# Optimization experiments

Hardware: AMD Instinct MI355X
Metric: run time of the kernel (lower is better)

Reference implementation:

```python
import jax, jax.numpy as jnp
import numpy as np

N = 50000      # nodes
E = 800000     # edges
HID = 64       # hidden_dim
HEADS = 4
DH = HID // HEADS
PIN = 128      # person_in_dim
DIN = 64       # disease_in_dim
NEXP = 4       # num_experts
K = 2          # topk
L = 2          # n_layers
NEG = 0.2      # gat_neg_slope


def setup_inputs() -> dict:
    key = jax.random.key(0)
    ks = iter(jax.random.split(key, 64))
    nrm = lambda shp, s=0.05: jax.random.normal(next(ks), shp, jnp.float32) * s
    d = {}
    d["features"] = jax.random.normal(next(ks), (N, PIN), jnp.float32)
    d["node_types"] = jax.random.randint(next(ks), (N,), 0, 2)
    d["src"] = jax.random.randint(next(ks), (E,), 0, N)
    d["dst"] = jax.random.randint(next(ks), (E,), 0, N)
    d["W_person"] = nrm((PIN, HID)); d["b_person"] = jnp.zeros((HID,), jnp.float32)
    d["W_disease"] = nrm((DIN, HID)); d["b_disease"] = jnp.zeros((HID,), jnp.float32)
    d["gat_W"] = nrm((L, HID, HID)); d["gat_al"] = nrm((L, HEADS, DH)); d["gat_ar"] = nrm((L, HEADS, DH))
    d["gin_eps"] = jnp.zeros((L,), jnp.float32)
    d["gin_W1"] = nrm((L, HID, HID)); d["gin_b1"] = jnp.zeros((L, HID), jnp.float32)
    d["gin_W2"] = nrm((L, HID, HID)); d["gin_b2"] = jnp.zeros((L, HID), jnp.float32)
    for p in ("gat", "gin"):
        d[p + "_gW"] = nrm((HID, NEXP)); d[p + "_gb"] = jnp.zeros((NEXP,), jnp.float32)
        d[p + "_eW1"] = nrm((NEXP, HID, HID // 2)); d[p + "_eb1"] = jnp.zeros((NEXP, HID // 2), jnp.float32)
        d[p + "_eW2"] = nrm((NEXP, HID // 2, HID)); d[p + "_eb2"] = jnp.zeros((NEXP, HID), jnp.float32)
    d["fg_W1"] = nrm((2 * HID, HID)); d["fg_b1"] = jnp.zeros((HID,), jnp.float32)
    d["fg_W2"] = nrm((HID, HID)); d["fg_b2"] = jnp.zeros((HID,), jnp.float32)
    return d


def _edge_softmax(logits, dst):
    m = jax.ops.segment_max(logits, dst, num_segments=N)
    e = jnp.exp(logits - m[dst])
    s = jax.ops.segment_sum(e, dst, num_segments=N)
    return e / (s[dst] + 1e-9)


def _gat(h, src, dst, gat_W, gat_al, gat_ar):
    for l in range(L):
        hW = (h @ gat_W[l]).reshape(N, HEADS, DH)
        el = (hW * gat_al[l]).sum(-1)                    # [N, HEADS]
        er = (hW * gat_ar[l]).sum(-1)
        lg = jax.nn.leaky_relu(el[src] + er[dst], NEG)   # [E, HEADS]
        a = _edge_softmax(lg, dst)
        out = jax.ops.segment_sum(hW[src] * a[:, :, None], dst, num_segments=N)
        h2 = out.reshape(N, HID) + h                     # residual=True
        h = jax.nn.relu(h2) if l < L - 1 else h2
    return h


def _gin(h, src, dst, gin_eps, gin_W1, gin_b1, gin_W2, gin_b2):
    deg = jax.ops.segment_sum(jnp.ones((E,), jnp.float32), dst, num_segments=N)
    inv = 1.0 / jnp.maximum(deg, 1.0)
    for l in range(L):
        agg = jax.ops.segment_sum(h[src], dst, num_segments=N) * inv[:, None]  # 'mean' aggregator
        x = (1.0 + gin_eps[l]) * h + agg                 # learn_eps=True
        x = jax.nn.relu(x @ gin_W1[l] + gin_b1[l]) @ gin_W2[l] + gin_b2[l]     # 2-layer MLP
        h = jax.nn.relu(x) if l < L - 1 else x
    return h


def _expert(h, gW, gb, eW1, eb1, eW2, eb2):
    probs = jax.nn.softmax(h @ gW + gb, axis=-1)         # [N, NEXP]
    topv, topi = jax.lax.top_k(probs, K)
    topv = topv / topv.sum(-1, keepdims=True)
    hot = jax.nn.one_hot(topi, NEXP, dtype=h.dtype)      # [N, K, NEXP]
    w = (hot * topv[..., None]).sum(1)                   # [N, NEXP] sparse weights
    e1 = jax.nn.relu(jnp.einsum('nd,edh->neh', h, eW1) + eb1)
    e2 = jnp.einsum('neh,ehd->ned', e1, eW2) + eb2       # [N, NEXP, HID]
    out = (e2 * w[:, :, None]).sum(1)
    f = hot.sum(1).mean(0)                               # routed fraction per expert
    P = probs.mean(0)
    aux = NEXP * jnp.sum(f * P)                          # switch-style load balancing
    return out, aux


def reference(features, node_types, src, dst, W_person, b_person, W_disease, b_disease,
              gat_W, gat_al, gat_ar, gin_eps, gin_W1, gin_b1, gin_W2, gin_b2,
              gat_gW, gat_gb, gat_eW1, gat_eb1, gat_eW2, gat_eb2,
              gin_gW, gin_gb, gin_eW1, gin_eb1, gin_eW2, gin_eb2,
              fg_W1, fg_b1, fg_W2, fg_b2):
    # per-type projection + scatter into shared buffer
    hp = features[:, :PIN] @ W_person + b_person
    hd = features[:, :DIN] @ W_disease + b_disease
    h = jnp.where((node_types == 0)[:, None], hp, hd)
    z_gat = _gat(h, src, dst, gat_W, gat_al, gat_ar)
    z_gin = _gin(h, src, dst, gin_eps, gin_W1, gin_b1, gin_W2, gin_b2)
    zg, aux_g = _expert(z_gat, gat_gW, gat_gb, gat_eW1, gat_eb1, gat_eW2, gat_eb2)
    zi, aux_i = _expert(z_gin, gin_gW, gin_gb, gin_eW1, gin_eb1, gin_eW2, gin_eb2)
    z = zi * zg
    u = jnp.concatenate([zg, zi], axis=-1)
    gate = jax.nn.sigmoid(jax.nn.relu(u @ fg_W1 + fg_b1) @ fg_W2 + fg_b2)
    u_prime = gate  # source calls fusion_gate(u) twice -> identical deterministic value
    z = gate * z + (1.0 - gate) * u_prime
    return z, aux_i + aux_g
```

## Files before the change

kernel.cpp:

```cpp
#include <hip/hip_runtime.h>

#define NN 50000
#define EE 800000
#define NEG 0.2f
#define NBG 391
#define NBE 196
#define NBKT 391
#define EPB 4096
#define NSEG 196

typedef __attribute__((ext_vector_type(8))) short s8;
typedef __attribute__((ext_vector_type(4))) float f4;

__device__ __forceinline__ float leaky(float x) { return x > 0.f ? x : NEG * x; }
__device__ __forceinline__ unsigned bf16r(float x) {
    unsigned u = __float_as_uint(x);
    return (u + 0x7fffu + ((u >> 16) & 1u)) >> 16;
}
__device__ __forceinline__ float lo16(unsigned p) { return __uint_as_float(p << 16); }
__device__ __forceinline__ float hi16(unsigned p) { return __uint_as_float(p & 0xffff0000u); }

__device__ __forceinline__ s8 a_from_f32(const float* p) {
    float4 u = *reinterpret_cast<const float4*>(p);
    float4 v = *reinterpret_cast<const float4*>(p + 4);
    s8 r;
    r[0] = (short)bf16r(u.x); r[1] = (short)bf16r(u.y);
    r[2] = (short)bf16r(u.z); r[3] = (short)bf16r(u.w);
    r[4] = (short)bf16r(v.x); r[5] = (short)bf16r(v.y);
    r[6] = (short)bf16r(v.z); r[7] = (short)bf16r(v.w);
    return r;
}

__global__ __launch_bounds__(256) void k_binA_pre(
        const int* __restrict__ src, const int* __restrict__ dst,
        int* __restrict__ seg_off, int* __restrict__ seg_cnt,
        unsigned* __restrict__ gseg, int* __restrict__ bucket_tot,
        const float* __restrict__ feat, const int* __restrict__ types,
        const float* __restrict__ Wp, const float* __restrict__ bp,
        const float* __restrict__ Wd, const float* __restrict__ bd,
        const float* __restrict__ gW, const float* __restrict__ al,
        const float* __restrict__ ar,
        float* __restrict__ h0f, unsigned* __restrict__ P,
        float* __restrict__ el, float* __restrict__ er) {
    __shared__ unsigned short WpT[64 * 136];
    __shared__ unsigned short WdT[64 * 72];
    __shared__ unsigned short WgT[64 * 72];
    __shared__ unsigned short y0s[4][16 * 72];
    if (blockIdx.x < NSEG) {
        unsigned* sbuf = (unsigned*)WpT;
        int* cnt = (int*)WdT;
        int* pre = (int*)WgT;
        int* ssc = (int*)y0s;
        for (int i = threadIdx.x; i < NBKT; i += 256) cnt[i] = 0;
        __syncthreads();
        int e0 = blockIdx.x * EPB;
        int nE = EE - e0; if (nE > EPB) nE = EPB;
        int b[16]; unsigned val[16]; int rk[16];
        #pragma unroll
        for (int i = 0; i < 16; i++) {
            int li = i * 256 + threadIdx.x;
            if (li < nE) {
                int e = e0 + li;
                int d = dst[e], s = src[e];
                b[i] = d >> 7;
                val[i] = ((unsigned)s << 7) | (unsigned)(d & 127);
                rk[i] = atomicAdd(&cnt[b[i]], 1);
            } else b[i] = -1;
        }
        __syncthreads();
        int t = threadIdx.x;
        int c0 = (2 * t     < NBKT) ? cnt[2 * t]     : 0;
        int c1 = (2 * t + 1 < NBKT) ? cnt[2 * t + 1] : 0;
        ssc[t] = c0 + c1;
        __syncthreads();
        for (int off = 1; off < 256; off <<= 1) {
            int u = (t >= off) ? ssc[t - off] : 0;
            __syncthreads();
            ssc[t] += u;
            __syncthreads();
        }
        int base = ssc[t] - (c0 + c1);
        pre[2 * t] = base;
        pre[2 * t + 1] = base + c0;
        __syncthreads();
        #pragma unroll
        for (int i = 0; i < 16; i++)
            if (b[i] >= 0) sbuf[pre[b[i]] + rk[i]] = val[i];
        for (int i = t; i < NBKT; i += 256) {
            seg_off[blockIdx.x * NBKT + i] = pre[i];
            seg_cnt[blockIdx.x * NBKT + i] = cnt[i];
            atomicAdd(&bucket_tot[i], cnt[i]);
        }
        __syncthreads();
        for (int i = t; i < nE; i += 256)
            gseg[(size_t)blockIdx.x * EPB + i] = sbuf[i];
        return;
    }
    for (int idx = threadIdx.x; idx < 128 * 64; idx += 256) {
        int k = idx >> 6, n = idx & 63;
        WpT[n * 136 + k] = (unsigned short)bf16r(Wp[idx]);
    }
    for (int idx = threadIdx.x; idx < 64 * 64; idx += 256) {
        int k = idx >> 6, n = idx & 63;
        WdT[n * 72 + k] = (unsigned short)bf16r(Wd[idx]);
        WgT[n * 72 + k] = (unsigned short)bf16r(gW[idx]);
    }
    __syncthreads();
    int wv = threadIdx.x >> 6, lane = threadIdx.x & 63;
    int quad = lane >> 4, l16 = lane & 15;
    int gw2 = (blockIdx.x - NSEG) * 4 + wv;
    int mtEnd = gw2 * 2 + 2; if (mtEnd > 3125) mtEnd = 3125;
    for (int mt = gw2 * 2; mt < mtEnd; mt++) {
        int row0 = mt * 16;
        const float* arow = feat + (size_t)(row0 + l16) * 128;
        f4 accp[4], accd[4];
        #pragma unroll
        for (int t = 0; t < 4; t++) { accp[t] = f4{0.f,0.f,0.f,0.f}; accd[t] = f4{0.f,0.f,0.f,0.f}; }
        #pragma unroll
        for (int ks = 0; ks < 4; ks++) {
            s8 a = a_from_f32(arow + ks * 32 + quad * 8);
            #pragma unroll
            for (int t = 0; t < 4; t++) {
                s8 b = *(const s8*)&WpT[(t * 16 + l16) * 136 + ks * 32 + quad * 8];
                accp[t] = __builtin_amdgcn_mfma_f32_16x16x32_bf16(a, b, accp[t], 0, 0, 0);
                if (ks < 2) {
                    s8 bd_ = *(const s8*)&WdT[(t * 16 + l16) * 72 + ks * 32 + quad * 8];
                    accd[t] = __builtin_amdgcn_mfma_f32_16x16x32_bf16(a, bd_, accd[t], 0, 0, 0);
                }
            }
        }
        int ty[4];
        #pragma unroll
        for (int r = 0; r < 4; r++) ty[r] = types[row0 + quad * 4 + r];
        float vv[4][4];
        #pragma unroll
        for (int t = 0; t < 4; t++) {
            int col = t * 16 + l16;
            float bpv = bp[col], bdv = bd[col];
            #pragma unroll
            for (int r = 0; r < 4; r++) {
                float v = ty[r] ? (accd[t][r] + bdv) : (accp[t][r] + bpv);
                vv[t][r] = v;
                h0f[(size_t)(row0 + quad * 4 + r) * 64 + col] = v;
                y0s[wv][(quad * 4 + r) * 72 + col] = (unsigned short)bf16r(v);
            }
        }
        s8 a0 = *(const s8*)&y0s[wv][l16 * 72 + quad * 8];
        s8 a1 = *(const s8*)&y0s[wv][l16 * 72 + 32 + quad * 8];
        f4 hw[4];
        #pragma unroll
        for (int t = 0; t < 4; t++) {
            hw[t] = f4{0.f,0.f,0.f,0.f};
            s8 b0 = *(const s8*)&WgT[(t * 16 + l16) * 72 + quad * 8];
            hw[t] = __builtin_amdgcn_mfma_f32_16x16x32_bf16(a0, b0, hw[t], 0, 0, 0);
            s8 b1_ = *(const s8*)&WgT[(t * 16 + l16) * 72 + 32 + quad * 8];
            hw[t] = __builtin_amdgcn_mfma_f32_16x16x32_bf16(a1, b1_, hw[t], 0, 0, 0);
        }
        #pragma unroll
        for (int t = 0; t < 4; t++) {
            int col = t * 16 + l16;
            float alv = al[col], arv = ar[col];
            #pragma unroll
            for (int r = 0; r < 4; r++) {
                int row = row0 + quad * 4 + r;
                float h = hw[t][r];
                P[(size_t)row * 64 + col] = bf16r(h) | (bf16r(vv[t][r]) << 16);
                float pl = h * alv, pr = h * arv;
                #pragma unroll
                for (int m = 1; m < 16; m <<= 1) {
                    pl += __shfl_xor(pl, m, 64);
                    pr += __shfl_xor(pr, m, 64);
                }
                if (l16 == 0) {
                    el[(size_t)row * 4 + t] = pl;
                    er[(size_t)row * 4 + t] = pr;
                }
            }
        }
    }
}

__global__ __launch_bounds__(256) void k_binB(
        int* __restrict__ row_start, const int* __restrict__ seg_off,
        const int* __restrict__ seg_cnt, const unsigned* __restrict__ gseg,
        int* __restrict__ csr_src, const int* __restrict__ bucket_tot) {
    __shared__ int spre[256];
    __shared__ int soff[NSEG];
    __shared__ int ss[256];
    __shared__ int kur[128];
    __shared__ int sred[4];
    int b = blockIdx.x;
    int t = threadIdx.x;
    int bt = 0;
    for (int i = t; i < b; i += 256) bt += bucket_tot[i];
    #pragma unroll
    for (int o2 = 1; o2 < 64; o2 <<= 1) bt += __shfl_xor(bt, o2, 64);
    if ((t & 63) == 0) sred[t >> 6] = bt;
    int c0 = (t < NSEG) ? seg_cnt[t * NBKT + b] : 0;
    if (t < NSEG) soff[t] = seg_off[t * NBKT + b];
    ss[t] = c0;
    __syncthreads();
    int bstart = sred[0] + sred[1] + sred[2] + sred[3];
    for (int off = 1; off < 256; off <<= 1) {
        int u = (t >= off) ? ss[t - off] : 0;
        __syncthreads();
        ss[t] += u;
        __syncthreads();
    }
    spre[t] = ss[t] - c0;
    int cntb = ss[255];
    if (t < 128) kur[t] = 0;
    __syncthreads();
    for (int idx = t; idx < cntb; idx += 256) {
        int lo = 0, hi = 255;
        #pragma unroll
        for (int s = 0; s < 8; s++) {
            int mid = (lo + hi + 1) >> 1;
            if (spre[mid] <= idx) lo = mid; else hi = mid - 1;
        }
        unsigned v = gseg[(size_t)lo * EPB + soff[lo] + (idx - spre[lo])];
        atomicAdd(&kur[v & 127], 1);
    }
    __syncthreads();
    int deg = (t < 128) ? kur[t] : 0;
    ss[t] = deg;
    __syncthreads();
    for (int off = 1; off < 256; off <<= 1) {
        int u = (t >= off) ? ss[t - off] : 0;
        __syncthreads();
        ss[t] += u;
        __syncthreads();
    }
    if (t < 128) {
        int cur = bstart + ss[t] - deg;
        kur[t] = cur;
        int d = (b << 7) + t;
        if (d < NN) row_start[d] = cur;
    }
    if (b == 0 && t == 0) row_start[NN] = EE;
    __syncthreads();
    for (int idx = t; idx < cntb; idx += 256) {
        int lo = 0, hi = 255;
        #pragma unroll
        for (int s = 0; s < 8; s++) {
            int mid = (lo + hi + 1) >> 1;
            if (spre[mid] <= idx) lo = mid; else hi = mid - 1;
        }
        unsigned v = gseg[(size_t)lo * EPB + soff[lo] + (idx - spre[lo])];
        int p = atomicAdd(&kur[v & 127], 1);
        csr_src[p] = (int)(v >> 7);
    }
}

template <int RELU>
__global__ void k_edges(const int* __restrict__ rows, const int* __restrict__ csr,
                        const unsigned* __restrict__ Pin,
                        const float* __restrict__ el, const float* __restrict__ er,
                        const float* __restrict__ gat_in, const float* __restrict__ gin_in,
                        const float* __restrict__ eps_p,
                        float* __restrict__ vgf, unsigned short* __restrict__ vgb,
                        unsigned short* __restrict__ xb) {
    __shared__ float ews[4][256];
    int wv = threadIdx.x >> 6, lane = threadIdx.x & 63;
    int n = blockIdx.x * 4 + wv;
    int st = rows[n], dg = rows[n + 1] - st;
    int hd = lane >> 4;
    float4 erv = *reinterpret_cast<const float4*>(er + (size_t)n * 4);
    float accg = 0.f, acci = 0.f, ssum = 0.f;
    for (int base = 0; base < dg; base += 64) {
        int rem = dg - base; if (rem > 64) rem = 64;
        int myi = 0;
        if (lane < rem) {
            myi = csr[st + base + lane];
            float4 lv = *reinterpret_cast<const float4*>(el + (size_t)myi * 4);
            float4 ev;
            ev.x = __expf(leaky(lv.x + erv.x));
            ev.y = __expf(leaky(lv.y + erv.y));
            ev.z = __expf(leaky(lv.z + erv.z));
            ev.w = __expf(leaky(lv.w + erv.w));
            *reinterpret_cast<float4*>(&ews[wv][lane * 4]) = ev;
        }
        int j = 0;
        for (; j + 4 <= rem; j += 4) {
            int s0 = __shfl(myi, j, 64),     s1 = __shfl(myi, j + 1, 64);
            int s2 = __shfl(myi, j + 2, 64), s3 = __shfl(myi, j + 3, 64);
            unsigned p0 = Pin[(size_t)s0 * 64 + lane];
            unsigned p1 = Pin[(size_t)s1 * 64 + lane];
            unsigned p2 = Pin[(size_t)s2 * 64 + lane];
            unsigned p3 = Pin[(size_t)s3 * 64 + lane];
            float a0 = ews[wv][(j + 0) * 4 + hd];
            float a1 = ews[wv][(j + 1) * 4 + hd];
            float a2 = ews[wv][(j + 2) * 4 + hd];
            float a3 = ews[wv][(j + 3) * 4 + hd];
            accg += a0 * lo16(p0) + a1 * lo16(p1) + a2 * lo16(p2) + a3 * lo16(p3);
            acci += hi16(p0) + hi16(p1) + hi16(p2) + hi16(p3);
            ssum += a0 + a1 + a2 + a3;
        }
        for (; j < rem; j++) {
            int s0 = __shfl(myi, j, 64);
            unsigned p0 = Pin[(size_t)s0 * 64 + lane];
            float a0 = ews[wv][j * 4 + hd];
            accg += a0 * lo16(p0); acci += hi16(p0); ssum += a0;
        }
    }
    float vg = accg / (ssum + 1e-9f) + gat_in[(size_t)n * 64 + lane];
    if (RELU) vg = fmaxf(vg, 0.f);
    float invd = 1.0f / fmaxf((float)dg, 1.0f);
    float x = (1.0f + eps_p[0]) * gin_in[(size_t)n * 64 + lane] + acci * invd;
    size_t off = (size_t)n * 64 + lane;
    vgf[off] = vg;
    vgb[off] = (unsigned short)bf16r(vg);
    xb[off] = (unsigned short)bf16r(x);
}

template <int L>
__global__ __launch_bounds__(256) void k_mlp(const unsigned short* __restrict__ Gx,
        const unsigned short* __restrict__ Eb,
        const float* __restrict__ W1, const float* __restrict__ b1,
        const float* __restrict__ W2, const float* __restrict__ b2,
        const float* __restrict__ gatW, const float* __restrict__ al,
        const float* __restrict__ ar,
        unsigned short* __restrict__ Fb, float* __restrict__ Cf,
        unsigned* __restrict__ P, float* __restrict__ el, float* __restrict__ er,
        const float* __restrict__ Zg, const float* __restrict__ ggW,
        const float* __restrict__ ggb, const float* __restrict__ igW,
        const float* __restrict__ igb,
        float* __restrict__ wgtg, float* __restrict__ wgti,
        float* __restrict__ stats) {
    __shared__ unsigned short W1T[64 * 72];
    __shared__ unsigned short W2T[64 * 72];
    __shared__ unsigned short WgT[(L == 0) ? 64 * 72 : 64];
    __shared__ unsigned short y1s[4][16 * 72];
    __shared__ float sstat[16];
    if (L == 1 && threadIdx.x < 16) sstat[threadIdx.x] = 0.f;
    for (int idx = threadIdx.x; idx < 64 * 64; idx += 256) {
        int k = idx >> 6, n = idx & 63;
        W1T[n * 72 + k] = (unsigned short)bf16r(W1[idx]);
        W2T[n * 72 + k] = (unsigned short)bf16r(W2[idx]);
        if (L == 0) WgT[n * 72 + k] = (unsigned short)bf16r(gatW[idx]);
    }
    __syncthreads();
    int wv = threadIdx.x >> 6, lane = threadIdx.x & 63;
    int quad = lane >> 4, l16 = lane & 15;
    int gw = blockIdx.x * 4 + wv;
    int mtEnd = gw * 2 + 2; if (mtEnd > 3125) mtEnd = 3125;
    float sp[2][4] = {{0,0,0,0},{0,0,0,0}};
    float sh[2][4] = {{0,0,0,0},{0,0,0,0}};
    for (int mt = gw * 2; mt < mtEnd; mt++) {
        int row0 = mt * 16;
        const unsigned short* arow = Gx + (size_t)(row0 + l16) * 64;
        s8 a0 = *(const s8*)(arow + quad * 8);
        s8 a1 = *(const s8*)(arow + 32 + quad * 8);
        f4 acc1[4];
        #pragma unroll
        for (int t = 0; t < 4; t++) {
            acc1[t] = f4{0.f,0.f,0.f,0.f};
            s8 b0 = *(const s8*)&W1T[(t * 16 + l16) * 72 + quad * 8];
            acc1[t] = __builtin_amdgcn_mfma_f32_16x16x32_bf16(a0, b0, acc1[t], 0, 0, 0);
            s8 b1_ = *(const s8*)&W1T[(t * 16 + l16) * 72 + 32 + quad * 8];
            acc1[t] = __builtin_amdgcn_mfma_f32_16x16x32_bf16(a1, b1_, acc1[t], 0, 0, 0);
        }
        #pragma unroll
        for (int t = 0; t < 4; t++) {
            float b1v = b1[t * 16 + l16];
            #pragma unroll
            for (int r = 0; r < 4; r++) {
                float v = fmaxf(acc1[t][r] + b1v, 0.f);
                y1s[wv][(quad * 4 + r) * 72 + t * 16 + l16] = (unsigned short)bf16r(v);
            }
        }
        s8 c0 = *(const s8*)&y1s[wv][l16 * 72 + quad * 8];
        s8 c1 = *(const s8*)&y1s[wv][l16 * 72 + 32 + quad * 8];
        f4 acc2[4];
        #pragma unroll
        for (int t = 0; t < 4; t++) {
            acc2[t] = f4{0.f,0.f,0.f,0.f};
            s8 b0 = *(const s8*)&W2T[(t * 16 + l16) * 72 + quad * 8];
            acc2[t] = __builtin_amdgcn_mfma_f32_16x16x32_bf16(c0, b0, acc2[t], 0, 0, 0);
            s8 b1_ = *(const s8*)&W2T[(t * 16 + l16) * 72 + 32 + quad * 8];
            acc2[t] = __builtin_amdgcn_mfma_f32_16x16x32_bf16(c1, b1_, acc2[t], 0, 0, 0);
        }
        unsigned short vb[4][4];
        float vout[4][4];
        #pragma unroll
        for (int t = 0; t < 4; t++) {
            int col = t * 16 + l16;
            float b2v = b2[col];
            #pragma unroll
            for (int r = 0; r < 4; r++) {
                float v = acc2[t][r] + b2v;
                if (L == 0) v = fmaxf(v, 0.f);
                size_t off = (size_t)(row0 + quad * 4 + r) * 64 + col;
                unsigned short vb16 = (unsigned short)bf16r(v);
                vb[t][r] = vb16;
                vout[t][r] = v;
                Fb[off] = vb16;
                if (L == 0) Cf[off] = v;
            }
        }
        if (L == 0) {
            const unsigned short* erow = Eb + (size_t)(row0 + l16) * 64;
            s8 e0 = *(const s8*)(erow + quad * 8);
            s8 e1 = *(const s8*)(erow + 32 + quad * 8);
            f4 hw[4];
            #pragma unroll
            for (int t = 0; t < 4; t++) {
                hw[t] = f4{0.f,0.f,0.f,0.f};
                s8 b0 = *(const s8*)&WgT[(t * 16 + l16) * 72 + quad * 8];
                hw[t] = __builtin_amdgcn_mfma_f32_16x16x32_bf16(e0, b0, hw[t], 0, 0, 0);
                s8 b1_ = *(const s8*)&WgT[(t * 16 + l16) * 72 + 32 + quad * 8];
                hw[t] = __builtin_amdgcn_mfma_f32_16x16x32_bf16(e1, b1_, hw[t], 0, 0, 0);
            }
            #pragma unroll
            for (int t = 0; t < 4; t++) {
                int col = t * 16 + l16;
                float alv = al[col], arv = ar[col];
                #pragma unroll
                for (int r = 0; r < 4; r++) {
                    int row = row0 + quad * 4 + r;
                    float h = hw[t][r];
                    P[(size_t)row * 64 + col] = bf16r(h) | ((unsigned)vb[t][r] << 16);
                    float pl = h * alv, pr = h * arv;
                    #pragma unroll
                    for (int m = 1; m < 16; m <<= 1) {
                        pl += __shfl_xor(pl, m, 64);
                        pr += __shfl_xor(pr, m, 64);
                    }
                    if (l16 == 0) {
                        el[(size_t)row * 4 + t] = pl;
                        er[(size_t)row * 4 + t] = pr;
                    }
                }
            }
        } else {
            #pragma unroll
            for (int r = 0; r < 4; r++) {
                int row = row0 + quad * 4 + r;
                float pg[4] = {0,0,0,0}, pi[4] = {0,0,0,0};
                #pragma unroll
                for (int t = 0; t < 4; t++) {
                    int col = t * 16 + l16;
                    float zgv = Zg[(size_t)row * 64 + col];
                    float ziv = vout[t][r];
                    #pragma unroll
                    for (int e = 0; e < 4; e++) {
                        pg[e] += zgv * ggW[col * 4 + e];
                        pi[e] += ziv * igW[col * 4 + e];
                    }
                }
                #pragma unroll
                for (int m = 1; m < 16; m <<= 1) {
                    #pragma unroll
                    for (int e = 0; e < 4; e++) {
                        pg[e] += __shfl_xor(pg[e], m, 64);
                        pi[e] += __shfl_xor(pi[e], m, 64);
                    }
                }
                if (l16 == 0) {
                    #pragma unroll
                    for (int q = 0; q < 2; q++) {
                        float lg0 = (q ? pi[0] + igb[0] : pg[0] + ggb[0]);
                        float lg1 = (q ? pi[1] + igb[1] : pg[1] + ggb[1]);
                        float lg2 = (q ? pi[2] + igb[2] : pg[2] + ggb[2]);
                        float lg3 = (q ? pi[3] + igb[3] : pg[3] + ggb[3]);
                        float mx = fmaxf(fmaxf(lg0, lg1), fmaxf(lg2, lg3));
                        float ex0 = __expf(lg0 - mx), ex1 = __expf(lg1 - mx);
                        float ex2 = __expf(lg2 - mx), ex3 = __expf(lg3 - mx);
                        float inv = 1.0f / (ex0 + ex1 + ex2 + ex3);
                        float pr4[4] = {ex0 * inv, ex1 * inv, ex2 * inv, ex3 * inv};
                        int i1 = 0; float v1 = pr4[0];
                        #pragma unroll
                        for (int t = 1; t < 4; t++) if (pr4[t] > v1) { v1 = pr4[t]; i1 = t; }
                        int i2 = -1; float v2 = -1.f;
                        #pragma unroll
                        for (int t = 0; t < 4; t++) if (t != i1 && pr4[t] > v2) { v2 = pr4[t]; i2 = t; }
                        float wsum = v1 + v2;
                        float wq[4] = {0.f, 0.f, 0.f, 0.f};
                        wq[i1] = v1 / wsum; wq[i2] = v2 / wsum;
                        float* WD = q ? wgti : wgtg;
                        *reinterpret_cast<float4*>(WD + (size_t)row * 4) =
                            float4{wq[0], wq[1], wq[2], wq[3]};
                        #pragma unroll
                        for (int t = 0; t < 4; t++) sp[q][t] += pr4[t];
                        sh[q][i1] += 1.f; sh[q][i2] += 1.f;
                    }
                }
            }
        }
    }
    if (L == 1) {
        __syncthreads();
        if (l16 == 0) {
            #pragma unroll
            for (int q = 0; q < 2; q++)
                #pragma unroll
                for (int e = 0; e < 4; e++) {
                    atomicAdd(&sstat[q * 8 + e], sp[q][e]);
                    atomicAdd(&sstat[q * 8 + 4 + e], sh[q][e]);
                }
        }
        __syncthreads();
        if (threadIdx.x < 16) atomicAdd(&stats[threadIdx.x], sstat[threadIdx.x]);
    }
}

__global__ __launch_bounds__(256) void k_expert(const unsigned short* __restrict__ Eb,
        const unsigned short* __restrict__ Fb,
        const float* __restrict__ g_eW1, const float* __restrict__ g_eb1,
        const float* __restrict__ g_eW2, const float* __restrict__ g_eb2,
        const float* __restrict__ i_eW1, const float* __restrict__ i_eb1,
        const float* __restrict__ i_eW2, const float* __restrict__ i_eb2,
        const float* __restrict__ wgtg, const float* __restrict__ wgti,
        float* __restrict__ moegf, float* __restrict__ moeif,
        unsigned short* __restrict__ ub) {
    __shared__ unsigned short w1t[4 * 32 * 72];
    __shared__ unsigned short w2t[4 * 64 * 40];
    __shared__ unsigned short y1s[4][16 * 40];
    int p = (blockIdx.x >= NBE) ? 1 : 0;
    int bb = blockIdx.x - p * NBE;
    const unsigned short* Ab = p ? Fb : Eb;
    const float* eW1 = p ? i_eW1 : g_eW1;
    const float* eb1 = p ? i_eb1 : g_eb1;
    const float* eW2 = p ? i_eW2 : g_eW2;
    const float* eb2 = p ? i_eb2 : g_eb2;
    const float* wgt = p ? wgti : wgtg;
    float* moef = p ? moeif : moegf;
    int qoff = p ? 64 : 0;
    for (int g = threadIdx.x; g < 8192; g += 256) {
        int e = g >> 11, rem = g & 2047;
        int k = rem >> 5, n = rem & 31;
        w1t[e * 2304 + n * 72 + k] = (unsigned short)bf16r(eW1[g]);
    }
    for (int g = threadIdx.x; g < 8192; g += 256) {
        int e = g >> 11, rem = g & 2047;
        int k = rem >> 6, n = rem & 63;
        w2t[e * 2560 + n * 40 + k] = (unsigned short)bf16r(eW2[g]);
    }
    __syncthreads();
    int wv = threadIdx.x >> 6, lane = threadIdx.x & 63;
    int quad = lane >> 4, l16 = lane & 15;
    int gw = bb * 4 + wv;
    int mtEnd = gw * 4 + 4; if (mtEnd > 3125) mtEnd = 3125;
    for (int mt = gw * 4; mt < mtEnd; mt++) {
        int row0 = mt * 16;
        const unsigned short* arow = Ab + (size_t)(row0 + l16) * 64;
        s8 a0 = *(const s8*)(arow + quad * 8);
        s8 a1 = *(const s8*)(arow + 32 + quad * 8);
        f4 outacc[4];
        #pragma unroll
        for (int t = 0; t < 4; t++) outacc[t] = f4{0.f,0.f,0.f,0.f};
        for (int e = 0; e < 4; e++) {
            f4 acc1[2];
            #pragma unroll
            for (int t = 0; t < 2; t++) {
                acc1[t] = f4{0.f,0.f,0.f,0.f};
                s8 b0 = *(const s8*)&w1t[e * 2304 + (t * 16 + l16) * 72 + quad * 8];
                acc1[t] = __builtin_amdgcn_mfma_f32_16x16x32_bf16(a0, b0, acc1[t], 0, 0, 0);
                s8 b1_ = *(const s8*)&w1t[e * 2304 + (t * 16 + l16) * 72 + 32 + quad * 8];
                acc1[t] = __builtin_amdgcn_mfma_f32_16x16x32_bf16(a1, b1_, acc1[t], 0, 0, 0);
            }
            #pragma unroll
            for (int t = 0; t < 2; t++) {
                float b1v = eb1[e * 32 + t * 16 + l16];
                #pragma unroll
                for (int r = 0; r < 4; r++) {
                    float v = fmaxf(acc1[t][r] + b1v, 0.f);
                    y1s[wv][(quad * 4 + r) * 40 + t * 16 + l16] = (unsigned short)bf16r(v);
                }
            }
            s8 a2 = *(const s8*)&y1s[wv][l16 * 40 + quad * 8];
            f4 acc2[4];
            #pragma unroll
            for (int t = 0; t < 4; t++) {
                acc2[t] = f4{0.f,0.f,0.f,0.f};
                s8 b2_ = *(const s8*)&w2t[e * 2560 + (t * 16 + l16) * 40 + quad * 8];
                acc2[t] = __builtin_amdgcn_mfma_f32_16x16x32_bf16(a2, b2_, acc2[t], 0, 0, 0);
            }
            #pragma unroll
            for (int t = 0; t < 4; t++) {
                float b2v = eb2[e * 64 + t * 16 + l16];
                #pragma unroll
                for (int r = 0; r < 4; r++) {
                    float we = wgt[(size_t)(row0 + quad * 4 + r) * 4 + e];
                    outacc[t][r] += we * (acc2[t][r] + b2v);
                }
            }
        }
        #pragma unroll
        for (int t = 0; t < 4; t++) {
            int col = t * 16 + l16;
            #pragma unroll
            for (int r = 0; r < 4; r++) {
                int row = row0 + quad * 4 + r;
                float v = outacc[t][r];
                moef[(size_t)row * 64 + col] = v;
                ub[(size_t)row * 128 + qoff + col] = (unsigned short)bf16r(v);
            }
        }
    }
}

__global__ __launch_bounds__(256) void k_fusion(const unsigned short* __restrict__ ubuf,
        const float* __restrict__ W1, const float* __restrict__ b1,
        const float* __restrict__ W2, const float* __restrict__ b2,
        const float* __restrict__ moegf, const float* __restrict__ moeif,
        float* __restrict__ out, const float* __restrict__ stats) {
    __shared__ unsigned short W1T[64 * 136];
    __shared__ unsigned short W2T[64 * 72];
    __shared__ unsigned short y1s[4][16 * 72];
    for (int idx = threadIdx.x; idx < 128 * 64; idx += 256) {
        int k = idx >> 6, n = idx & 63;
        W1T[n * 136 + k] = (unsigned short)bf16r(W1[idx]);
    }
    for (int idx = threadIdx.x; idx < 64 * 64; idx += 256) {
        int k = idx >> 6, n = idx & 63;
        W2T[n * 72 + k] = (unsigned short)bf16r(W2[idx]);
    }
    __syncthreads();
    int wv = threadIdx.x >> 6, lane = threadIdx.x & 63;
    int quad = lane >> 4, l16 = lane & 15;
    int gw = blockIdx.x * 4 + wv;
    int mtEnd = gw * 2 + 2; if (mtEnd > 3125) mtEnd = 3125;
    for (int mt = gw * 2; mt < mtEnd; mt++) {
        int row0 = mt * 16;
        const unsigned short* arow = ubuf + (size_t)(row0 + l16) * 128;
        f4 acc1[4];
        #pragma unroll
        for (int t = 0; t < 4; t++) acc1[t] = f4{0.f,0.f,0.f,0.f};
        #pragma unroll
        for (int ks = 0; ks < 4; ks++) {
            s8 a = *(const s8*)(arow + ks * 32 + quad * 8);
            #pragma unroll
            for (int t = 0; t < 4; t++) {
                s8 b = *(const s8*)&W1T[(t * 16 + l16) * 136 + ks * 32 + quad * 8];
                acc1[t] = __builtin_amdgcn_mfma_f32_16x16x32_bf16(a, b, acc1[t], 0, 0, 0);
            }
        }
        #pragma unroll
        for (int t = 0; t < 4; t++) {
            float b1v = b1[t * 16 + l16];
            #pragma unroll
            for (int r = 0; r < 4; r++) {
                float v = fmaxf(acc1[t][r] + b1v, 0.f);
                y1s[wv][(quad * 4 + r) * 72 + t * 16 + l16] = (unsigned short)bf16r(v);
            }
        }
        f4 acc2[4];
        #pragma unroll
        for (int t = 0; t < 4; t++) acc2[t] = f4{0.f,0.f,0.f,0.f};
        #pragma unroll
        for (int ks = 0; ks < 2; ks++) {
            s8 a = *(const s8*)&y1s[wv][l16 * 72 + ks * 32 + quad * 8];
            #pragma unroll
            for (int t = 0; t < 4; t++) {
                s8 b = *(const s8*)&W2T[(t * 16 + l16) * 72 + ks * 32 + quad * 8];
                acc2[t] = __builtin_amdgcn_mfma_f32_16x16x32_bf16(a, b, acc2[t], 0, 0, 0);
            }
        }
        #pragma unroll
        for (int t = 0; t < 4; t++) {
            int col = t * 16 + l16;
            float b2v = b2[col];
            #pragma unroll
            for (int r = 0; r < 4; r++) {
                int row = row0 + quad * 4 + r;
                float g = 1.0f / (1.0f + __expf(-(acc2[t][r] + b2v)));
                float zgv = moegf[(size_t)row * 64 + col];
                float ziv = moeif[(size_t)row * 64 + col];
                out[(size_t)row * 64 + col] = g * zgv * ziv + (1.0f - g) * g;
            }
        }
    }
    if (blockIdx.x == 0 && threadIdx.x < 64) {
        int t = threadIdx.x;
        float s = (t < 16) ? stats[t] : 0.f;
        float aux = 0.f;
        for (int q = 0; q < 2; q++) {
            float a = 0.f;
            for (int e = 0; e < 4; e++) {
                float pr = __shfl(s, q * 8 + e, 64);
                float f  = __shfl(s, q * 8 + 4 + e, 64);
                a += (f / (float)NN) * (pr / (float)NN);
            }
            aux += 4.0f * a;
        }
        if (t == 0) out[(size_t)NN * 64] = aux;
    }
}

extern "C" void kernel_launch(void* const* d_in, const int* in_sizes, int n_in,
                              void* d_out, int out_size, void* d_ws, size_t ws_size,
                              hipStream_t stream) {
    (void)in_sizes; (void)n_in; (void)out_size; (void)ws_size;
    const float* features  = (const float*)d_in[0];
    const int*   node_types= (const int*)d_in[1];
    const int*   src       = (const int*)d_in[2];
    const int*   dst       = (const int*)d_in[3];
    const float* W_person  = (const float*)d_in[4];
    const float* b_person  = (const float*)d_in[5];
    const float* W_disease = (const float*)d_in[6];
    const float* b_disease = (const float*)d_in[7];
    const float* gat_W     = (const float*)d_in[8];
    const float* gat_al    = (const float*)d_in[9];
    const float* gat_ar    = (const float*)d_in[10];
    const float* gin_eps   = (const float*)d_in[11];
    const float* gin_W1    = (const float*)d_in[12];
    const float* gin_b1    = (const float*)d_in[13];
    const float* gin_W2    = (const float*)d_in[14];
    const float* gin_b2    = (const float*)d_in[15];
    const float* gat_gW    = (const float*)d_in[16];
    const float* gat_gb    = (const float*)d_in[17];
    const float* gat_eW1   = (const float*)d_in[18];
    const float* gat_eb1   = (const float*)d_in[19];
    const float* gat_eW2   = (const float*)d_in[20];
    const float* gat_eb2   = (const float*)d_in[21];
    const float* gin_gW    = (const float*)d_in[22];
    const float* gin_gb    = (const float*)d_in[23];
    const float* gin_eW1   = (const float*)d_in[24];
    const float* gin_eb1   = (const float*)d_in[25];
    const float* gin_eW2   = (const float*)d_in[26];
    const float* gin_eb2   = (const float*)d_in[27];
    const float* fg_W1     = (const float*)d_in[28];
    const float* fg_b1     = (const float*)d_in[29];
    const float* fg_W2     = (const float*)d_in[30];
    const float* fg_b2     = (const float*)d_in[31];
    float* out = (float*)d_out;

    float* ws = (float*)d_ws;
    size_t o = 0;
    float* A = ws + o; o += (size_t)NN * 64;
    float* B = ws + o; o += (size_t)NN * 64;
    float* C = ws + o; o += (size_t)NN * 64;
    unsigned short* E  = (unsigned short*)(ws + o); o += (size_t)NN * 32;
    unsigned short* F  = (unsigned short*)(ws + o); o += (size_t)NN * 32;
    unsigned short* G  = (unsigned short*)(ws + o); o += (size_t)NN * 32;
    unsigned* P = (unsigned*)(ws + o); o += (size_t)NN * 64;
    float* el = ws + o; o += (size_t)NN * 4;
    float* er = ws + o; o += (size_t)NN * 4;
    float* wgtg = ws + o; o += (size_t)NN * 4;
    float* wgti = ws + o; o += (size_t)NN * 4;
    int* bucket_tot = (int*)(ws + o); o += 392;
    float* stats    = ws + o; o += 16;
    int* row_start = (int*)(ws + o); o += NN + 4;
    int* csr_src   = (int*)(ws + o); o += EE;
    int* seg_off   = (int*)(ws + o); o += NSEG * NBKT + 64;
    int* seg_cnt   = (int*)(ws + o); o += NSEG * NBKT + 64;
    unsigned* gseg = (unsigned*)(ws + o); o += (size_t)NSEG * EPB;

    unsigned short* ub = (unsigned short*)A;

    const int NB_node = NN / 4;

    hipMemsetAsync(bucket_tot, 0, sizeof(int) * 392 + sizeof(float) * 16, stream);

    k_binA_pre<<<NSEG + NBG, 256, 0, stream>>>(src, dst, seg_off, seg_cnt, gseg, bucket_tot,
                                               features, node_types, W_person, b_person,
                                               W_disease, b_disease, gat_W, gat_al, gat_ar,
                                               A, P, el, er);

    k_binB<<<NBKT, 256, 0, stream>>>(row_start, seg_off, seg_cnt, gseg, csr_src, bucket_tot);

    k_edges<1><<<NB_node, 256, 0, stream>>>(row_start, csr_src, P, el, er, A, A,
                                            gin_eps, B, E, G);
    k_mlp<0><<<NBG, 256, 0, stream>>>(G, E, gin_W1, gin_b1, gin_W2, gin_b2,
                                      gat_W + 4096, gat_al + 64, gat_ar + 64,
                                      F, C, P, el, er,
                                      nullptr, nullptr, nullptr, nullptr, nullptr,
                                      nullptr, nullptr, nullptr);

    k_edges<0><<<NB_node, 256, 0, stream>>>(row_start, csr_src, P, el, er, B, C,
                                            gin_eps + 1, B, E, G);
    k_mlp<1><<<NBG, 256, 0, stream>>>(G, nullptr, gin_W1 + 4096, gin_b1 + 64,
                                      gin_W2 + 4096, gin_b2 + 64,
                                      nullptr, nullptr, nullptr,
                                      F, nullptr, nullptr, nullptr, nullptr,
                                      B, gat_gW, gat_gb, gin_gW, gin_gb,
                                      wgtg, wgti, stats);

    k_expert<<<NBE * 2, 256, 0, stream>>>(E, F,
                                          gat_eW1, gat_eb1, gat_eW2, gat_eb2,
                                          gin_eW1, gin_eb1, gin_eW2, gin_eb2,
                                          wgtg, wgti, B, C, ub);

    k_fusion<<<NBG, 256, 0, stream>>>(ub, fg_W1, fg_b1, fg_W2, fg_b2, B, C, out, stats);
}
```

Before: 320.3 us.

## Fuse MoE expert and fusion-gate kernels into one tail kernel

Merges the expert kernel and the fusion-gate kernel into a single launch. Each wave computes both experts' outputs for its two row tiles, keeps them in registers, and writes only the bf16 concatenation buffer, which the same wave reads back for the gate MLP. This removes one launch and the fp32 round trip of the expert outputs through global memory. In exchange, each block now converts all three weight sets into shared memory in turn, which adds barriers and more per-block setup work, and it raises register pressure from holding the expert accumulators.

```diff
diff --git a/kernel.cpp b/kernel.cpp
--- a/kernel.cpp
+++ b/kernel.cpp
@@ -4,7 +4,7 @@
 #define EE 800000
 #define NEG 0.2f
 #define NBG 391
-#define NBE 196
+#define NBT 392
 #define NBKT 391
 #define EPB 4096
 #define NSEG 196
@@ -504,170 +504,169 @@
     }
 }
 
-__global__ __launch_bounds__(256) void k_expert(const unsigned short* __restrict__ Eb,
+__global__ __launch_bounds__(256) void k_tail(const unsigned short* __restrict__ Eb,
         const unsigned short* __restrict__ Fb,
         const float* __restrict__ g_eW1, const float* __restrict__ g_eb1,
         const float* __restrict__ g_eW2, const float* __restrict__ g_eb2,
         const float* __restrict__ i_eW1, const float* __restrict__ i_eb1,
         const float* __restrict__ i_eW2, const float* __restrict__ i_eb2,
         const float* __restrict__ wgtg, const float* __restrict__ wgti,
-        float* __restrict__ moegf, float* __restrict__ moeif,
-        unsigned short* __restrict__ ub) {
-    __shared__ unsigned short w1t[4 * 32 * 72];
-    __shared__ unsigned short w2t[4 * 64 * 40];
-    __shared__ unsigned short y1s[4][16 * 40];
-    int p = (blockIdx.x >= NBE) ? 1 : 0;
-    int bb = blockIdx.x - p * NBE;
-    const unsigned short* Ab = p ? Fb : Eb;
-    const float* eW1 = p ? i_eW1 : g_eW1;
-    const float* eb1 = p ? i_eb1 : g_eb1;
-    const float* eW2 = p ? i_eW2 : g_eW2;
-    const float* eb2 = p ? i_eb2 : g_eb2;
-    const float* wgt = p ? wgti : wgtg;
-    float* moef = p ? moeif : moegf;
-    int qoff = p ? 64 : 0;
-    for (int g = threadIdx.x; g < 8192; g += 256) {
-        int e = g >> 11, rem = g & 2047;
-        int k = rem >> 5, n = rem & 31;
-        w1t[e * 2304 + n * 72 + k] = (unsigned short)bf16r(eW1[g]);
-    }
-    for (int g = threadIdx.x; g < 8192; g += 256) {
-        int e = g >> 11, rem = g & 2047;
-        int k = rem >> 6, n = rem & 63;
-        w2t[e * 2560 + n * 40 + k] = (unsigned short)bf16r(eW2[g]);
-    }
-    __syncthreads();
-    int wv = threadIdx.x >> 6, lane = threadIdx.x & 63;
-    int quad = lane >> 4, l16 = lane & 15;
-    int gw = bb * 4 + wv;
-    int mtEnd = gw * 4 + 4; if (mtEnd > 3125) mtEnd = 3125;
-    for (int mt = gw * 4; mt < mtEnd; mt++) {
-        int row0 = mt * 16;
-        const unsigned short* arow = Ab + (size_t)(row0 + l16) * 64;
-        s8 a0 = *(const s8*)(arow + quad * 8);
-        s8 a1 = *(const s8*)(arow + 32 + quad * 8);
-        f4 outacc[4];
-        #pragma unroll
-        for (int t = 0; t < 4; t++) outacc[t] = f4{0.f,0.f,0.f,0.f};
-        for (int e = 0; e < 4; e++) {
-            f4 acc1[2];
-            #pragma unroll
-            for (int t = 0; t < 2; t++) {
-                acc1[t] = f4{0.f,0.f,0.f,0.f};
-                s8 b0 = *(const s8*)&w1t[e * 2304 + (t * 16 + l16) * 72 + quad * 8];
-                acc1[t] = __builtin_amdgcn_mfma_f32_16x16x32_bf16(a0, b0, acc1[t], 0, 0, 0);
-                s8 b1_ = *(const s8*)&w1t[e * 2304 + (t * 16 + l16) * 72 + 32 + quad * 8];
-                acc1[t] = __builtin_amdgcn_mfma_f32_16x16x32_bf16(a1, b1_, acc1[t], 0, 0, 0);
-            }
-            #pragma unroll
-            for (int t = 0; t < 2; t++) {
-                float b1v = eb1[e * 32 + t * 16 + l16];
-                #pragma unroll
-                for (int r = 0; r < 4; r++) {
-                    float v = fmaxf(acc1[t][r] + b1v, 0.f);
-                    y1s[wv][(quad * 4 + r) * 40 + t * 16 + l16] = (unsigned short)bf16r(v);
-                }
-            }
-            s8 a2 = *(const s8*)&y1s[wv][l16 * 40 + quad * 8];
-            f4 acc2[4];
-            #pragma unroll
-            for (int t = 0; t < 4; t++) {
-                acc2[t] = f4{0.f,0.f,0.f,0.f};
-                s8 b2_ = *(const s8*)&w2t[e * 2560 + (t * 16 + l16) * 40 + quad * 8];
-                acc2[t] = __builtin_amdgcn_mfma_f32_16x16x32_bf16(a2, b2_, acc2[t], 0, 0, 0);
-            }
-            #pragma unroll
-            for (int t = 0; t < 4; t++) {
-                float b2v = eb2[e * 64 + t * 16 + l16];
-                #pragma unroll
-                for (int r = 0; r < 4; r++) {
-                    float we = wgt[(size_t)(row0 + quad * 4 + r) * 4 + e];
-                    outacc[t][r] += we * (acc2[t][r] + b2v);
-                }
-            }
-        }
-        #pragma unroll
-        for (int t = 0; t < 4; t++) {
-            int col = t * 16 + l16;
-            #pragma unroll
-            for (int r = 0; r < 4; r++) {
-                int row = row0 + quad * 4 + r;
-                float v = outacc[t][r];
-                moef[(size_t)row * 64 + col] = v;
-                ub[(size_t)row * 128 + qoff + col] = (unsigned short)bf16r(v);
-            }
-        }
-    }
-}
-
-__global__ __launch_bounds__(256) void k_fusion(const unsigned short* __restrict__ ubuf,
         const float* __restrict__ W1, const float* __restrict__ b1,
         const float* __restrict__ W2, const float* __restrict__ b2,
-        const float* __restrict__ moegf, const float* __restrict__ moeif,
-        float* __restrict__ out, const float* __restrict__ stats) {
-    __shared__ unsigned short W1T[64 * 136];
-    __shared__ unsigned short W2T[64 * 72];
+        unsigned short* __restrict__ ub, float* __restrict__ out,
+        const float* __restrict__ stats) {
+    __shared__ unsigned short wbuf[4 * 32 * 72 + 4 * 64 * 40];
     __shared__ unsigned short y1s[4][16 * 72];
-    for (int idx = threadIdx.x; idx < 128 * 64; idx += 256) {
-        int k = idx >> 6, n = idx & 63;
-        W1T[n * 136 + k] = (unsigned short)bf16r(W1[idx]);
-    }
-    for (int idx = threadIdx.x; idx < 64 * 64; idx += 256) {
-        int k = idx >> 6, n = idx & 63;
-        W2T[n * 72 + k] = (unsigned short)bf16r(W2[idx]);
-    }
-    __syncthreads();
     int wv = threadIdx.x >> 6, lane = threadIdx.x & 63;
     int quad = lane >> 4, l16 = lane & 15;
     int gw = blockIdx.x * 4 + wv;
-    int mtEnd = gw * 2 + 2; if (mtEnd > 3125) mtEnd = 3125;
-    for (int mt = gw * 2; mt < mtEnd; mt++) {
-        int row0 = mt * 16;
-        const unsigned short* arow = ubuf + (size_t)(row0 + l16) * 128;
-        f4 acc1[4];
-        #pragma unroll
-        for (int t = 0; t < 4; t++) acc1[t] = f4{0.f,0.f,0.f,0.f};
-        #pragma unroll
-        for (int ks = 0; ks < 4; ks++) {
-            s8 a = *(const s8*)(arow + ks * 32 + quad * 8);
+    int mt0 = gw * 2;
+    f4 moe[2][2][4];
+    #pragma unroll
+    for (int p = 0; p < 2; p++)
+        #pragma unroll
+        for (int m = 0; m < 2; m++)
+            #pragma unroll
+            for (int t = 0; t < 4; t++) moe[p][m][t] = f4{0.f,0.f,0.f,0.f};
+    #pragma unroll
+    for (int p = 0; p < 2; p++) {
+        const unsigned short* Ab = p ? Fb : Eb;
+        const float* eW1 = p ? i_eW1 : g_eW1;
+        const float* eb1 = p ? i_eb1 : g_eb1;
+        const float* eW2 = p ? i_eW2 : g_eW2;
+        const float* eb2 = p ? i_eb2 : g_eb2;
+        const float* wgt = p ? wgti : wgtg;
+        int qoff = p ? 64 : 0;
+        if (p) __syncthreads();
+        for (int g = threadIdx.x; g < 8192; g += 256) {
+            int e = g >> 11, rem = g & 2047;
+            int k = rem >> 5, n = rem & 31;
+            wbuf[e * 2304 + n * 72 + k] = (unsigned short)bf16r(eW1[g]);
+        }
+        for (int g = threadIdx.x; g < 8192; g += 256) {
+            int e = g >> 11, rem = g & 2047;
+            int k = rem >> 6, n = rem & 63;
+            wbuf[9216 + e * 2560 + n * 40 + k] = (unsigned short)bf16r(eW2[g]);
+        }
+        __syncthreads();
+        #pragma unroll
+        for (int m = 0; m < 2; m++) {
+            int mt = mt0 + m;
+            if (mt < 3125) {
+                int row0 = mt * 16;
+                const unsigned short* arow = Ab + (size_t)(row0 + l16) * 64;
+                s8 a0 = *(const s8*)(arow + quad * 8);
+                s8 a1 = *(const s8*)(arow + 32 + quad * 8);
+                for (int e = 0; e < 4; e++) {
+                    f4 acc1[2];
+                    #pragma unroll
+                    for (int t = 0; t < 2; t++) {
+                        acc1[t] = f4{0.f,0.f,0.f,0.f};
+                        s8 b0 = *(const s8*)&wbuf[e * 2304 + (t * 16 + l16) * 72 + quad * 8];
+                        acc1[t] = __builtin_amdgcn_mfma_f32_16x16x32_bf16(a0, b0, acc1[t], 0, 0, 0);
+                        s8 b1_ = *(const s8*)&wbuf[e * 2304 + (t * 16 + l16) * 72 + 32 + quad * 8];
+                        acc1[t] = __builtin_amdgcn_mfma_f32_16x16x32_bf16(a1, b1_, acc1[t], 0, 0, 0);
+                    }
+                    #pragma unroll
+                    for (int t = 0; t < 2; t++) {
+                        float b1v = eb1[e * 32 + t * 16 + l16];
+                        #pragma unroll
+                        for (int r = 0; r < 4; r++) {
+                            float v = fmaxf(acc1[t][r] + b1v, 0.f);
+                            y1s[wv][(quad * 4 + r) * 40 + t * 16 + l16] = (unsigned short)bf16r(v);
+                        }
+                    }
+                    s8 a2 = *(const s8*)&y1s[wv][l16 * 40 + quad * 8];
+                    f4 acc2[4];
+                    #pragma unroll
+                    for (int t = 0; t < 4; t++) {
+                        acc2[t] = f4{0.f,0.f,0.f,0.f};
+                        s8 b2_ = *(const s8*)&wbuf[9216 + e * 2560 + (t * 16 + l16) * 40 + quad * 8];
+                        acc2[t] = __builtin_amdgcn_mfma_f32_16x16x32_bf16(a2, b2_, acc2[t], 0, 0, 0);
+                    }
+                    #pragma unroll
+                    for (int t = 0; t < 4; t++) {
+                        float b2v = eb2[e * 64 + t * 16 + l16];
+                        #pragma unroll
+                        for (int r = 0; r < 4; r++) {
+                            float we = wgt[(size_t)(row0 + quad * 4 + r) * 4 + e];
+                            moe[p][m][t][r] += we * (acc2[t][r] + b2v);
+                        }
+                    }
+                }
+                #pragma unroll
+                for (int t = 0; t < 4; t++) {
+                    int col = t * 16 + l16;
+                    #pragma unroll
+                    for (int r = 0; r < 4; r++) {
+                        int row = row0 + quad * 4 + r;
+                        ub[(size_t)row * 128 + qoff + col] = (unsigned short)bf16r(moe[p][m][t][r]);
+                    }
+                }
+            }
+        }
+    }
+    __syncthreads();
+    for (int idx = threadIdx.x; idx < 128 * 64; idx += 256) {
+        int k = idx >> 6, n = idx & 63;
+        wbuf[n * 136 + k] = (unsigned short)bf16r(W1[idx]);
+    }
+    for (int idx = threadIdx.x; idx < 64 * 64; idx += 256) {
+        int k = idx >> 6, n = idx & 63;
+        wbuf[8704 + n * 72 + k] = (unsigned short)bf16r(W2[idx]);
+    }
+    __syncthreads();
+    #pragma unroll
+    for (int m = 0; m < 2; m++) {
+        int mt = mt0 + m;
+        if (mt < 3125) {
+            int row0 = mt * 16;
+            const unsigned short* arow = ub + (size_t)(row0 + l16) * 128;
+            f4 acc1[4];
+            #pragma unroll
+            for (int t = 0; t < 4; t++) acc1[t] = f4{0.f,0.f,0.f,0.f};
+            #pragma unroll
+            for (int ks = 0; ks < 4; ks++) {
+                s8 a = *(const s8*)(arow + ks * 32 + quad * 8);
+                #pragma unroll
+                for (int t = 0; t < 4; t++) {
+                    s8 b = *(const s8*)&wbuf[(t * 16 + l16) * 136 + ks * 32 + quad * 8];
+                    acc1[t] = __builtin_amdgcn_mfma_f32_16x16x32_bf16(a, b, acc1[t], 0, 0, 0);
+                }
+            }
             #pragma unroll
             for (int t = 0; t < 4; t++) {
-                s8 b = *(const s8*)&W1T[(t * 16 + l16) * 136 + ks * 32 + quad * 8];
-                acc1[t] = __builtin_amdgcn_mfma_f32_16x16x32_bf16(a, b, acc1[t], 0, 0, 0);
-            }
-        }
-        #pragma unroll
-        for (int t = 0; t < 4; t++) {
-            float b1v = b1[t * 16 + l16];
-            #pragma unroll
-            for (int r = 0; r < 4; r++) {
-                float v = fmaxf(acc1[t][r] + b1v, 0.f);
-                y1s[wv][(quad * 4 + r) * 72 + t * 16 + l16] = (unsigned short)bf16r(v);
-            }
-        }
-        f4 acc2[4];
-        #pragma unroll
-        for (int t = 0; t < 4; t++) acc2[t] = f4{0.f,0.f,0.f,0.f};
-        #pragma unroll
-        for (int ks = 0; ks < 2; ks++) {
-            s8 a = *(const s8*)&y1s[wv][l16 * 72 + ks * 32 + quad * 8];
+                float b1v = b1[t * 16 + l16];
+                #pragma unroll
+                for (int r = 0; r < 4; r++) {
+                    float v = fmaxf(acc1[t][r] + b1v, 0.f);
+                    y1s[wv][(quad * 4 + r) * 72 + t * 16 + l16] = (unsigned short)bf16r(v);
+                }
+            }
+            f4 acc2[4];
+            #pragma unroll
+            for (int t = 0; t < 4; t++) acc2[t] = f4{0.f,0.f,0.f,0.f};
+            #pragma unroll
+            for (int ks = 0; ks < 2; ks++) {
+                s8 a = *(const s8*)&y1s[wv][l16 * 72 + ks * 32 + quad * 8];
+                #pragma unroll
+                for (int t = 0; t < 4; t++) {
+                    s8 b = *(const s8*)&wbuf[8704 + (t * 16 + l16) * 72 + ks * 32 + quad * 8];
+                    acc2[t] = __builtin_amdgcn_mfma_f32_16x16x32_bf16(a, b, acc2[t], 0, 0, 0);
+                }
+            }
             #pragma unroll
             for (int t = 0; t < 4; t++) {
-                s8 b = *(const s8*)&W2T[(t * 16 + l16) * 72 + ks * 32 + quad * 8];
-                acc2[t] = __builtin_amdgcn_mfma_f32_16x16x32_bf16(a, b, acc2[t], 0, 0, 0);
-            }
-        }
-        #pragma unroll
-        for (int t = 0; t < 4; t++) {
-            int col = t * 16 + l16;
-            float b2v = b2[col];
-            #pragma unroll
-            for (int r = 0; r < 4; r++) {
-                int row = row0 + quad * 4 + r;
-                float g = 1.0f / (1.0f + __expf(-(acc2[t][r] + b2v)));
-                float zgv = moegf[(size_t)row * 64 + col];
-                float ziv = moeif[(size_t)row * 64 + col];
-                out[(size_t)row * 64 + col] = g * zgv * ziv + (1.0f - g) * g;
+                int col = t * 16 + l16;
+                float b2v = b2[col];
+                #pragma unroll
+                for (int r = 0; r < 4; r++) {
+                    int row = row0 + quad * 4 + r;
+                    float g = 1.0f / (1.0f + __expf(-(acc2[t][r] + b2v)));
+                    float zgv = moe[0][m][t][r];
+                    float ziv = moe[1][m][t][r];
+                    out[(size_t)row * 64 + col] = g * zgv * ziv + (1.0f - g) * g;
+                }
             }
         }
     }
@@ -777,10 +776,9 @@
                                       B, gat_gW, gat_gb, gin_gW, gin_gb,
                                       wgtg, wgti, stats);
 
-    k_expert<<<NBE * 2, 256, 0, stream>>>(E, F,
-                                          gat_eW1, gat_eb1, gat_eW2, gat_eb2,
-                                          gin_eW1, gin_eb1, gin_eW2, gin_eb2,
-                                          wgtg, wgti, B, C, ub);
-
-    k_fusion<<<NBG, 256, 0, stream>>>(ub, fg_W1, fg_b1, fg_W2, fg_b2, B, C, out, stats);
+    k_tail<<<NBT, 256, 0, stream>>>(E, F,
+                                    gat_eW1, gat_eb1, gat_eW2, gat_eb2,
+                                    gin_eW1, gin_eb1, gin_eW2, gin_eb2,
+                                    wgtg, wgti, fg_W1, fg_b1, fg_W2, fg_b2,
+                                    ub, out, stats);
 }
```

New measurement: 316.4 us, median of 3. About the same (-1.2%).
